# Performance work log

Hardware: AMD Instinct MI355X
Metric: run time of the kernel (lower is better)

The kernel has to match this reference:

```python
import jax, jax.numpy as jnp
import numpy as np

D_MODEL = 4096
NUM_EXPERTS = 64
TOP_K = 2


def setup_inputs() -> dict:
    key = jax.random.key(0)
    kx, kw, kb = jax.random.split(key, 3)
    x = jax.random.normal(kx, (4, 4096, D_MODEL), dtype=jnp.float32)
    # nn.Linear(d_model, num_experts): weight [E, D], bias [E]
    bound = 1.0 / np.sqrt(D_MODEL)
    W = jax.random.uniform(kw, (NUM_EXPERTS, D_MODEL), dtype=jnp.float32, minval=-bound, maxval=bound)
    b = jax.random.uniform(kb, (NUM_EXPERTS,), dtype=jnp.float32, minval=-bound, maxval=bound)
    return {"x": x, "W": W, "b": b}


def reference(x, W, b):
    # logits = gate(x): [B, S, E]
    logits = jnp.einsum("bsd,ed->bse", x, W) + b
    scores = jax.nn.softmax(logits, axis=-1)
    topk_scores, topk_idx = jax.lax.top_k(scores, TOP_K)  # [B,S,K]
    # scatter top-k scores back into a dense [B,S,E] dispatch mask
    onehot = jax.nn.one_hot(topk_idx, NUM_EXPERTS, dtype=scores.dtype)  # [B,S,K,E]
    dispatch_mask = jnp.einsum("bske,bsk->bse", onehot, topk_scores)
    return dispatch_mask
```

## Files before the change

kernel.cpp:

```cpp
#include <hip/hip_runtime.h>
#include <hip/hip_bf16.h>
#include <math.h>
#include <stdint.h>

#define DM 4096
#define NEXP 64
#define BK 64
#define NCH (DM / BK)
#define TOKW 32
#define KSPLIT 8
#define CHPS (NCH / KSPLIT)

typedef short bf16x8 __attribute__((ext_vector_type(8)));
typedef float f32x4  __attribute__((ext_vector_type(4)));

__device__ __forceinline__ void split2(float f0, float f1, uint32_t& hw, uint32_t& lw) {
    float2 ff; ff.x = f0; ff.y = f1;
    __hip_bfloat162 h = __float22bfloat162_rn(ff);
    union { __hip_bfloat162 b; uint32_t u; } ch; ch.b = h;
    hw = ch.u;
    float h0 = __bfloat162float(h.x);
    float h1 = __bfloat162float(h.y);
    float2 gg; gg.x = f0 - h0; gg.y = f1 - h1;
    __hip_bfloat162 l = __float22bfloat162_rn(gg);
    union { __hip_bfloat162 b; uint32_t u; } cl; cl.b = l;
    lw = cl.u;
}

__global__ __launch_bounds__(512) void wsplit_kernel(const float* __restrict__ W,
                                                     char* __restrict__ blob) {
    const int c   = blockIdx.x;
    const int tid = threadIdx.x;
    const int e   = tid >> 3;
    const int g   = tid & 7;

    const float* src = W + (size_t)e * DM + c * BK + g * 8;
    float x[8];
    *(float4*)(x)     = *(const float4*)(src);
    *(float4*)(x + 4) = *(const float4*)(src + 4);

    uint32_t hiw[4], low[4];
#pragma unroll
    for (int j = 0; j < 4; ++j) split2(x[2 * j], x[2 * j + 1], hiw[j], low[j]);

    const int ks = g >> 2;
    const int ln = (e & 15) | ((g & 3) << 4);
    const int n4 = e >> 4;
    const size_t base = (size_t)c * 16384 + (size_t)ks * 4096 + (size_t)n4 * 1024 + (size_t)ln * 16;
    *(uint4*)(blob + base)        = *(uint4*)hiw;
    *(uint4*)(blob + base + 8192) = *(uint4*)low;
}

__global__ __launch_bounds__(512, 4) void router_mfma_kernel(
    const float* __restrict__ X,
    const char* __restrict__ blob,
    const float* __restrict__ Bv,
    float* __restrict__ out)
{
    __shared__ float part[KSPLIT][TOKW][NEXP];

    const int tid  = threadIdx.x;
    const int lane = tid & 63;
    const int wv   = tid >> 6;
    const long tok0 = (long)blockIdx.x * TOKW;

    const int tk = lane & 15;
    const int kg = lane >> 4;

    const float* a0 = X + (size_t)(tok0 + tk) * DM + (size_t)wv * (CHPS * BK) + kg * 8;
    const float* a1 = a0 + (size_t)16 * DM;
    const char*  bw = blob + (size_t)(wv * CHPS) * 16384;

    f32x4 acc[2][4];
#pragma unroll
    for (int m = 0; m < 2; ++m)
#pragma unroll
        for (int n = 0; n < 4; ++n) acc[m][n] = (f32x4)0.0f;

    float xr[2][2][8];

    auto loadA = [&](int ci) {
#pragma unroll
        for (int m = 0; m < 2; ++m) {
            const float* am = (m == 0) ? a0 : a1;
#pragma unroll
            for (int ks = 0; ks < 2; ++ks) {
                const float* p = am + ci * BK + ks * 32;
                *(float4*)(xr[m][ks])     = *(const float4*)(p);
                *(float4*)(xr[m][ks] + 4) = *(const float4*)(p + 4);
            }
        }
    };

    loadA(0);
#pragma unroll 1
    for (int ci = 0; ci < CHPS; ++ci) {
        bf16x8 ah[2][2], al[2][2];
#pragma unroll
        for (int m = 0; m < 2; ++m)
#pragma unroll
            for (int ks = 0; ks < 2; ++ks) {
                uint32_t hw[4], lw[4];
#pragma unroll
                for (int j = 0; j < 4; ++j)
                    split2(xr[m][ks][2 * j], xr[m][ks][2 * j + 1], hw[j], lw[j]);
                ah[ks][m] = *(bf16x8*)hw;
                al[ks][m] = *(bf16x8*)lw;
            }

        if (ci + 1 < CHPS) loadA(ci + 1);

        const char* bb = bw + (size_t)ci * 16384;
#pragma unroll
        for (int ks = 0; ks < 2; ++ks) {
#pragma unroll
            for (int n = 0; n < 4; ++n) {
                const size_t bo = (size_t)ks * 4096 + (size_t)n * 1024 + (size_t)lane * 16;
                bf16x8 bh = *(const bf16x8*)(bb + bo);
                bf16x8 bl = *(const bf16x8*)(bb + 8192 + bo);
#pragma unroll
                for (int m = 0; m < 2; ++m) {
                    acc[m][n] = __builtin_amdgcn_mfma_f32_16x16x32_bf16(ah[ks][m], bh, acc[m][n], 0, 0, 0);
                    acc[m][n] = __builtin_amdgcn_mfma_f32_16x16x32_bf16(ah[ks][m], bl, acc[m][n], 0, 0, 0);
                    acc[m][n] = __builtin_amdgcn_mfma_f32_16x16x32_bf16(al[ks][m], bh, acc[m][n], 0, 0, 0);
                    acc[m][n] = __builtin_amdgcn_mfma_f32_16x16x32_bf16(al[ks][m], bl, acc[m][n], 0, 0, 0);
                }
            }
        }
    }

#pragma unroll
    for (int m = 0; m < 2; ++m)
#pragma unroll
        for (int n = 0; n < 4; ++n)
#pragma unroll
            for (int r = 0; r < 4; ++r)
                part[wv][m * 16 + kg * 4 + r][n * 16 + tk] = acc[m][n][r];
    __syncthreads();

#pragma unroll
    for (int i = 0; i < 4; ++i) {
        const int cell = tid + i * 512;
        const int t = cell >> 6;
        const int e = cell & 63;
        float s = part[0][t][e];
#pragma unroll
        for (int w = 1; w < KSPLIT; ++w) s += part[w][t][e];
        part[0][t][e] = s;
    }
    __syncthreads();

    const float bias = Bv[lane];
#pragma unroll 1
    for (int j = 0; j < TOKW / KSPLIT; ++j) {
        const int t = wv * (TOKW / KSPLIT) + j;
        float v = part[0][t][lane] + bias;

        float m1 = v;        int i1 = lane;
        float m2 = -3.4e38f; int i2 = 127;
#pragma unroll
        for (int s = 1; s < 64; s <<= 1) {
            float om1 = __shfl_xor(m1, s, 64);
            int   oi1 = __shfl_xor(i1, s, 64);
            float om2 = __shfl_xor(m2, s, 64);
            int   oi2 = __shfl_xor(i2, s, 64);
            bool bw2 = (om1 > m1) || (om1 == m1 && oi1 < i1);
            float l1v = bw2 ? m1 : om1;  int l1i = bw2 ? i1 : oi1;
            float w2v = bw2 ? om2 : m2;  int w2i = bw2 ? oi2 : i2;
            if (bw2) { m1 = om1; i1 = oi1; }
            bool tw = (l1v > w2v) || (l1v == w2v && l1i < w2i);
            m2 = tw ? l1v : w2v;  i2 = tw ? l1i : w2i;
        }

        float p = expf(v - m1);
        float ssum = p;
#pragma unroll
        for (int s = 1; s < 64; s <<= 1) ssum += __shfl_xor(ssum, s, 64);

        float sc = (lane == i1 || lane == i2) ? (p / ssum) : 0.0f;
        out[(size_t)(tok0 + t) * NEXP + lane] = sc;
    }
}

extern "C" void kernel_launch(void* const* d_in, const int* in_sizes, int n_in,
                              void* d_out, int out_size, void* d_ws, size_t ws_size,
                              hipStream_t stream) {
    const float* X  = (const float*)d_in[0];
    const float* W  = (const float*)d_in[1];
    const float* Bv = (const float*)d_in[2];
    float* out = (float*)d_out;

    char* blob = (char*)d_ws;
    wsplit_kernel<<<dim3(NCH), dim3(512), 0, stream>>>(W, blob);

    const int n_tokens = 4 * 4096;
    router_mfma_kernel<<<dim3(n_tokens / TOKW), dim3(512), 0, stream>>>(X, blob, Bv, out);
}
```

Baseline: 77.25 us.

## Split router GEMM into K-group partial kernel with register-resident weights plus finalize

Restructures the router so each block owns one of 8 K-groups and keeps that group's split-bf16 weight fragments in registers while streaming 8 tiles of 16 tokens. Each tile's partial logits are reduced across waves in shared memory and written to a global workspace. A separate finalize kernel sums the 8 K-group partials and does the bias, top-2 and softmax. This is meant to stop reloading weights on every chunk and to improve parallelism, at the cost of an extra global round-trip for partials (about 32 MB written and read back) and one more kernel launch.

```diff
diff --git a/kernel.cpp b/kernel.cpp
--- a/kernel.cpp
+++ b/kernel.cpp
@@ -6,10 +6,11 @@
 #define DM 4096
 #define NEXP 64
 #define BK 64
-#define NCH (DM / BK)
-#define TOKW 32
-#define KSPLIT 8
-#define CHPS (NCH / KSPLIT)
+#define NCH 64
+#define KGRP 8
+#define TILE_T 16
+#define TILES_PB 8
+#define NTOK 16384
 
 typedef short bf16x8 __attribute__((ext_vector_type(8)));
 typedef float f32x4  __attribute__((ext_vector_type(4)));
@@ -51,119 +52,122 @@
     *(uint4*)(blob + base + 8192) = *(uint4*)low;
 }
 
-__global__ __launch_bounds__(512, 4) void router_mfma_kernel(
+__global__ __launch_bounds__(512, 4) void partial_kernel(
     const float* __restrict__ X,
     const char* __restrict__ blob,
+    float* __restrict__ pws)
+{
+    __shared__ float part[KGRP][TILE_T][66];
+
+    const int tid  = threadIdx.x;
+    const int lane = tid & 63;
+    const int wv   = tid >> 6;
+    const int b    = blockIdx.x;
+    const int g    = b & 7;
+    const long tokbase = (long)(b >> 3) * (TILES_PB * TILE_T);
+    const int c    = g * 8 + wv;
+
+    const char* bb = blob + (size_t)c * 16384;
+    bf16x8 bh[2][4], bl[2][4];
+#pragma unroll
+    for (int ks = 0; ks < 2; ++ks)
+#pragma unroll
+        for (int n = 0; n < 4; ++n) {
+            const size_t off = (size_t)ks * 4096 + (size_t)n * 1024 + (size_t)lane * 16;
+            bh[ks][n] = *(const bf16x8*)(bb + off);
+            bl[ks][n] = *(const bf16x8*)(bb + 8192 + off);
+        }
+
+    const int tk = lane & 15;
+    const int kg = lane >> 4;
+    const float* abase = X + (size_t)(tokbase + tk) * DM + c * BK + kg * 8;
+
+    float xr[2][8];
+    auto loadA = [&](int t) {
+        const float* p = abase + (size_t)t * TILE_T * DM;
+#pragma unroll
+        for (int ks = 0; ks < 2; ++ks) {
+            *(float4*)(xr[ks])     = *(const float4*)(p + ks * 32);
+            *(float4*)(xr[ks] + 4) = *(const float4*)(p + ks * 32 + 4);
+        }
+    };
+
+    loadA(0);
+#pragma unroll 1
+    for (int t = 0; t < TILES_PB; ++t) {
+        bf16x8 ah[2], al[2];
+#pragma unroll
+        for (int ks = 0; ks < 2; ++ks) {
+            uint32_t hw[4], lw[4];
+#pragma unroll
+            for (int j = 0; j < 4; ++j)
+                split2(xr[ks][2 * j], xr[ks][2 * j + 1], hw[j], lw[j]);
+            ah[ks] = *(bf16x8*)hw;
+            al[ks] = *(bf16x8*)lw;
+        }
+        if (t + 1 < TILES_PB) loadA(t + 1);
+
+        f32x4 acc[4];
+#pragma unroll
+        for (int n = 0; n < 4; ++n) acc[n] = (f32x4)0.0f;
+#pragma unroll
+        for (int ks = 0; ks < 2; ++ks)
+#pragma unroll
+            for (int n = 0; n < 4; ++n) {
+                acc[n] = __builtin_amdgcn_mfma_f32_16x16x32_bf16(ah[ks], bh[ks][n], acc[n], 0, 0, 0);
+                acc[n] = __builtin_amdgcn_mfma_f32_16x16x32_bf16(ah[ks], bl[ks][n], acc[n], 0, 0, 0);
+                acc[n] = __builtin_amdgcn_mfma_f32_16x16x32_bf16(al[ks], bh[ks][n], acc[n], 0, 0, 0);
+                acc[n] = __builtin_amdgcn_mfma_f32_16x16x32_bf16(al[ks], bl[ks][n], acc[n], 0, 0, 0);
+            }
+
+#pragma unroll
+        for (int n = 0; n < 4; ++n)
+#pragma unroll
+            for (int r = 0; r < 4; ++r)
+                part[wv][kg * 4 + r][n * 16 + tk] = acc[n][r];
+        __syncthreads();
+
+#pragma unroll
+        for (int i = 0; i < 2; ++i) {
+            const int cell = tid + i * 512;
+            const int t16 = cell >> 6;
+            const int e   = cell & 63;
+            float s = part[0][t16][e];
+#pragma unroll
+            for (int w = 1; w < KGRP; ++w) s += part[w][t16][e];
+            pws[((size_t)(tokbase + t * TILE_T + t16) * KGRP + g) * NEXP + e] = s;
+        }
+        __syncthreads();
+    }
+}
+
+__global__ __launch_bounds__(256) void finalize_kernel(
+    const float* __restrict__ pws,
     const float* __restrict__ Bv,
     float* __restrict__ out)
 {
-    __shared__ float part[KSPLIT][TOKW][NEXP];
-
     const int tid  = threadIdx.x;
     const int lane = tid & 63;
-    const int wv   = tid >> 6;
-    const long tok0 = (long)blockIdx.x * TOKW;
-
-    const int tk = lane & 15;
-    const int kg = lane >> 4;
-
-    const float* a0 = X + (size_t)(tok0 + tk) * DM + (size_t)wv * (CHPS * BK) + kg * 8;
-    const float* a1 = a0 + (size_t)16 * DM;
-    const char*  bw = blob + (size_t)(wv * CHPS) * 16384;
-
-    f32x4 acc[2][4];
-#pragma unroll
-    for (int m = 0; m < 2; ++m)
-#pragma unroll
-        for (int n = 0; n < 4; ++n) acc[m][n] = (f32x4)0.0f;
-
-    float xr[2][2][8];
-
-    auto loadA = [&](int ci) {
-#pragma unroll
-        for (int m = 0; m < 2; ++m) {
-            const float* am = (m == 0) ? a0 : a1;
-#pragma unroll
-            for (int ks = 0; ks < 2; ++ks) {
-                const float* p = am + ci * BK + ks * 32;
-                *(float4*)(xr[m][ks])     = *(const float4*)(p);
-                *(float4*)(xr[m][ks] + 4) = *(const float4*)(p + 4);
-            }
-        }
-    };
-
-    loadA(0);
+    const int wid  = blockIdx.x * 4 + (tid >> 6);
+    const float bias = Bv[lane];
+
 #pragma unroll 1
-    for (int ci = 0; ci < CHPS; ++ci) {
-        bf16x8 ah[2][2], al[2][2];
-#pragma unroll
-        for (int m = 0; m < 2; ++m)
-#pragma unroll
-            for (int ks = 0; ks < 2; ++ks) {
-                uint32_t hw[4], lw[4];
-#pragma unroll
-                for (int j = 0; j < 4; ++j)
-                    split2(xr[m][ks][2 * j], xr[m][ks][2 * j + 1], hw[j], lw[j]);
-                ah[ks][m] = *(bf16x8*)hw;
-                al[ks][m] = *(bf16x8*)lw;
-            }
-
-        if (ci + 1 < CHPS) loadA(ci + 1);
-
-        const char* bb = bw + (size_t)ci * 16384;
-#pragma unroll
-        for (int ks = 0; ks < 2; ++ks) {
-#pragma unroll
-            for (int n = 0; n < 4; ++n) {
-                const size_t bo = (size_t)ks * 4096 + (size_t)n * 1024 + (size_t)lane * 16;
-                bf16x8 bh = *(const bf16x8*)(bb + bo);
-                bf16x8 bl = *(const bf16x8*)(bb + 8192 + bo);
-#pragma unroll
-                for (int m = 0; m < 2; ++m) {
-                    acc[m][n] = __builtin_amdgcn_mfma_f32_16x16x32_bf16(ah[ks][m], bh, acc[m][n], 0, 0, 0);
-                    acc[m][n] = __builtin_amdgcn_mfma_f32_16x16x32_bf16(ah[ks][m], bl, acc[m][n], 0, 0, 0);
-                    acc[m][n] = __builtin_amdgcn_mfma_f32_16x16x32_bf16(al[ks][m], bh, acc[m][n], 0, 0, 0);
-                    acc[m][n] = __builtin_amdgcn_mfma_f32_16x16x32_bf16(al[ks][m], bl, acc[m][n], 0, 0, 0);
-                }
-            }
-        }
-    }
-
-#pragma unroll
-    for (int m = 0; m < 2; ++m)
-#pragma unroll
-        for (int n = 0; n < 4; ++n)
-#pragma unroll
-            for (int r = 0; r < 4; ++r)
-                part[wv][m * 16 + kg * 4 + r][n * 16 + tk] = acc[m][n][r];
-    __syncthreads();
-
-#pragma unroll
-    for (int i = 0; i < 4; ++i) {
-        const int cell = tid + i * 512;
-        const int t = cell >> 6;
-        const int e = cell & 63;
-        float s = part[0][t][e];
-#pragma unroll
-        for (int w = 1; w < KSPLIT; ++w) s += part[w][t][e];
-        part[0][t][e] = s;
-    }
-    __syncthreads();
-
-    const float bias = Bv[lane];
-#pragma unroll 1
-    for (int j = 0; j < TOKW / KSPLIT; ++j) {
-        const int t = wv * (TOKW / KSPLIT) + j;
-        float v = part[0][t][lane] + bias;
+    for (int j = 0; j < 4; ++j) {
+        const long tok = (long)wid * 4 + j;
+        const float* p = pws + (size_t)tok * (KGRP * NEXP) + lane;
+        float s = p[0];
+#pragma unroll
+        for (int g2 = 1; g2 < KGRP; ++g2) s += p[g2 * NEXP];
+        float v = s + bias;
 
         float m1 = v;        int i1 = lane;
         float m2 = -3.4e38f; int i2 = 127;
 #pragma unroll
-        for (int s = 1; s < 64; s <<= 1) {
-            float om1 = __shfl_xor(m1, s, 64);
-            int   oi1 = __shfl_xor(i1, s, 64);
-            float om2 = __shfl_xor(m2, s, 64);
-            int   oi2 = __shfl_xor(i2, s, 64);
+        for (int s2 = 1; s2 < 64; s2 <<= 1) {
+            float om1 = __shfl_xor(m1, s2, 64);
+            int   oi1 = __shfl_xor(i1, s2, 64);
+            float om2 = __shfl_xor(m2, s2, 64);
+            int   oi2 = __shfl_xor(i2, s2, 64);
             bool bw2 = (om1 > m1) || (om1 == m1 && oi1 < i1);
             float l1v = bw2 ? m1 : om1;  int l1i = bw2 ? i1 : oi1;
             float w2v = bw2 ? om2 : m2;  int w2i = bw2 ? oi2 : i2;
@@ -172,13 +176,13 @@
             m2 = tw ? l1v : w2v;  i2 = tw ? l1i : w2i;
         }
 
-        float p = expf(v - m1);
-        float ssum = p;
-#pragma unroll
-        for (int s = 1; s < 64; s <<= 1) ssum += __shfl_xor(ssum, s, 64);
-
-        float sc = (lane == i1 || lane == i2) ? (p / ssum) : 0.0f;
-        out[(size_t)(tok0 + t) * NEXP + lane] = sc;
+        float pexp = expf(v - m1);
+        float ssum = pexp;
+#pragma unroll
+        for (int s2 = 1; s2 < 64; s2 <<= 1) ssum += __shfl_xor(ssum, s2, 64);
+
+        float sc = (lane == i1 || lane == i2) ? (pexp / ssum) : 0.0f;
+        out[tok * NEXP + lane] = sc;
     }
 }
 
@@ -190,9 +194,13 @@
     const float* Bv = (const float*)d_in[2];
     float* out = (float*)d_out;
 
-    char* blob = (char*)d_ws;
+    char*  blob = (char*)d_ws;
+    float* pws  = (float*)((char*)d_ws + (1 << 20));
+
     wsplit_kernel<<<dim3(NCH), dim3(512), 0, stream>>>(W, blob);
 
-    const int n_tokens = 4 * 4096;
-    router_mfma_kernel<<<dim3(n_tokens / TOKW), dim3(512), 0, stream>>>(X, blob, Bv, out);
-}
+    const int nblocks = (NTOK / (TILES_PB * TILE_T)) * KGRP;
+    partial_kernel<<<dim3(nblocks), dim3(512), 0, stream>>>(X, blob, pws);
+
+    finalize_kernel<<<dim3(NTOK / (4 * 4)), dim3(256), 0, stream>>>(pws, Bv, out);
+}
```

Result: no change. 78.44 us (+1.5%).
